# Kernel tuning notes

Hardware: AMD Instinct MI355X
Metric: run time of the kernel (lower is better)

The kernel has to match this reference:

```python
import jax, jax.numpy as jnp
from jax import lax
import numpy as np

B, NW, L, E, H, V = 8192, 4, 16, 128, 128, 64  # batch, words/example, max chars, emsize, hidden, char vocab


def setup_inputs() -> dict:
    key = jax.random.key(0)
    ks = jax.random.split(key, 13)
    s = 0.05
    return {
        "word_ids": jax.random.randint(ks[0], (B, NW, L), 0, V, dtype=jnp.int32),
        "lengths": jax.random.randint(ks[1], (B, NW), 1, L + 1, dtype=jnp.int32),
        "emb_i": jax.random.normal(ks[2], (V, E), jnp.float32),
        "W_ih": jax.random.normal(ks[3], (4 * H, E), jnp.float32) * s,
        "W_hh": jax.random.normal(ks[4], (4 * H, H), jnp.float32) * s,
        "b_ih": jax.random.normal(ks[5], (4 * H,), jnp.float32) * s,
        "b_hh": jax.random.normal(ks[6], (4 * H,), jnp.float32) * s,
        "conv1_w": jax.random.normal(ks[7], (4, 1, 2, 2), jnp.float32) * 0.5,
        "conv1_b": jax.random.normal(ks[8], (4,), jnp.float32) * 0.1,
        "conv2_w": jax.random.normal(ks[9], (8, 4, 2, 2), jnp.float32) * 0.5,
        "conv2_b": jax.random.normal(ks[10], (8,), jnp.float32) * 0.1,
        "scorer_w": jax.random.normal(ks[11], (1, 2 * 2 * 8), jnp.float32) * 0.2,
        "scorer_b": jax.random.normal(ks[12], (1,), jnp.float32) * 0.1,
    }


def reference(word_ids, lengths, emb_i, W_ih, W_hh, b_ih, b_hh,
              conv1_w, conv1_b, conv2_w, conv2_b, scorer_w, scorer_b):
    Bx, NWx, Lx = word_ids.shape
    Hh = W_hh.shape[1]
    BN = Bx * NWx
    # char embeddings for all words, packed: [L, BN, E]
    xs = emb_i[word_ids.reshape(BN, Lx)].transpose(1, 0, 2)
    # ragged lengths -> per-step update mask [L, BN]
    mask = jnp.arange(Lx, dtype=lengths.dtype)[:, None] < lengths.reshape(-1)[None, :]
    h0 = jnp.zeros((BN, Hh), emb_i.dtype)

    def step(carry, xm):
        h, c = carry
        x_t, m = xm
        gates = x_t @ W_ih.T + b_ih + h @ W_hh.T + b_hh  # torch LSTMCell gate order i,f,g,o
        i, f, g, o = jnp.split(gates, 4, axis=-1)
        i = jax.nn.sigmoid(i); f = jax.nn.sigmoid(f)
        g = jnp.tanh(g); o = jax.nn.sigmoid(o)
        c_new = f * c + i * g
        h_new = o * jnp.tanh(c_new)
        m = m[:, None]
        return (jnp.where(m, h_new, h), jnp.where(m, c_new, c)), None

    (h, c), _ = lax.scan(step, (h0, h0), (xs, mask))
    # Model.encode returns the cell state c
    reps = c.reshape(Bx, NWx, Hh)

    # pairwise cosine similarity matrix [B, NW, NW]
    norms = jnp.sqrt(jnp.sum(reps * reps, axis=-1))
    dots = jnp.einsum('bih,bjh->bij', reps, reps)
    cos = dots / (norms[:, :, None] * norms[:, None, :])

    # tiny 2-layer CNN scorer on the NWxNW matrix (NCHW)
    dn = ('NCHW', 'OIHW', 'NCHW')
    x_img = cos[:, None, :, :]
    out = jax.nn.relu(lax.conv_general_dilated(x_img, conv1_w, (1, 1), 'VALID', dimension_numbers=dn)
                      + conv1_b[None, :, None, None])
    out = jax.nn.relu(lax.conv_general_dilated(out, conv2_w, (1, 1), 'VALID', dimension_numbers=dn)
                      + conv2_b[None, :, None, None])
    flat = out.reshape(Bx, -1)  # channel-major flatten matches torch .view
    score = flat @ scorer_w.T + scorer_b
    return jax.nn.sigmoid(score)  # [B, 1] discriminator prob
```

## Files before the change

kernel.cpp:

```cpp
#include <hip/hip_runtime.h>

#define BSZ    8192
#define NWRD   4
#define SEQL   16
#define HDIM   128
#define VOCAB  64
#define NSEQ   (BSZ * NWRD)
#define WGSEQ  32
#define UPB    80
#define BINCAP (UPB * WGSEQ)
#define NBLK   512
#define RSTR   136

#define AS1 __attribute__((address_space(1)))
#define AS3 __attribute__((address_space(3)))

typedef float    f32x4  __attribute__((ext_vector_type(4)));
typedef float    f32x16 __attribute__((ext_vector_type(16)));
typedef __bf16   bf16x8 __attribute__((ext_vector_type(8)));
typedef _Float16 f16x8  __attribute__((ext_vector_type(8)));
typedef int      i32x4  __attribute__((ext_vector_type(4)));

union AccU { f32x16 v; f32x4 q[4]; float f[16]; };

__device__ __forceinline__ unsigned short f2bf(float f) {
    unsigned int u = __builtin_bit_cast(unsigned int, f);
    return (unsigned short)((u + 0x7fff + ((u >> 16) & 1)) >> 16);
}
__device__ __forceinline__ float sigm(float x) {
    return __builtin_amdgcn_rcpf(1.f + __builtin_amdgcn_exp2f(x * -1.44269504f));
}

__global__ void prep4(const float* __restrict__ emb, const float* __restrict__ W_ih,
                      const float* __restrict__ b_ih, const float* __restrict__ b_hh,
                      const float* __restrict__ W_hh, const int* __restrict__ lengths,
                      unsigned short* __restrict__ P2H, unsigned short* __restrict__ WA,
                      int* __restrict__ perm, int* __restrict__ gh)
{
    __shared__ int lh[16], gbase[16];
    const int blk = blockIdx.x, tid = threadIdx.x;

    if (blk < 128) {
        int idx = blk * 256 + tid;
        int v = idx >> 9, g = (idx >> 7) & 3, j = idx & 127;
        int n = g * 128 + j;
        const f32x4* er = (const f32x4*)(emb  + v * 128);
        const f32x4* wr = (const f32x4*)(W_ih + n * 128);
        f32x4 s4 = er[0] * wr[0];
#pragma unroll
        for (int e = 1; e < 32; ++e) s4 += er[e] * wr[e];
        float s = s4.x + s4.y + s4.z + s4.w + b_ih[n] + b_hh[n];
        int wv = j >> 5, jr = j & 31;
        int d = jr & 3, hl = (jr >> 2) & 1, q = jr >> 3;
        int cc = g * 16 + wv * 4 + hl * 2 + (q >> 1);
        int F  = v * 512 + ((cc ^ (v & 7)) << 3) + (q & 1) * 4 + d;
        P2H[F] = __builtin_bit_cast(unsigned short, (_Float16)s);
    } else if (blk < 384) {
        int idx = (blk - 128) * 256 + tid;
        int jj = idx & 7, lane = (idx >> 3) & 63, kc = (idx >> 9) & 7, tt = idx >> 12;
        int wv = tt >> 2, g = tt & 3;
        int n = g * 128 + wv * 32 + (lane & 31);
        int k = kc * 16 + (lane >> 5) * 8 + jj;
        WA[idx] = f2bf(W_hh[n * 128 + k]);
    } else {
        if (tid < 16) lh[tid] = 0;
        __syncthreads();
        int i = (blk - 384) * 256 + tid;
        int b = 16 - lengths[i];
        int rank = atomicAdd(&lh[b], 1);
        __syncthreads();
        if (tid < 16) gbase[tid] = atomicAdd(&gh[tid], lh[tid]);
        __syncthreads();
        perm[b * BINCAP + gbase[b] + rank] = i;
    }
}

__global__ __launch_bounds__(256, 2) void lstm4(
    const int* __restrict__ word_ids, const int* __restrict__ perm,
    int* __restrict__ gh, const unsigned short* __restrict__ P2H,
    const unsigned short* __restrict__ WA, float* __restrict__ c_out)
{
    __shared__ __align__(16) unsigned short ptab[VOCAB * 512];
    __shared__ __align__(16) unsigned short hbuf[2][WGSEQ * 128];

    const int tid    = threadIdx.x;
    const int wv     = tid >> 6;
    const int lane   = tid & 63;
    const int lane31 = lane & 31;
    const int hl     = lane >> 5;

    {
        const char* src = (const char*)P2H;
        char*       dst = (char*)ptab;
#pragma unroll
        for (int r = 0; r < 16; ++r) {
            const int off = r * 4096 + wv * 1024;
            __builtin_amdgcn_global_load_lds(
                (const AS1 unsigned int*)(src + off + lane * 16),
                (AS3 unsigned int*)(dst + off), 16, 0, 0);
        }
    }

    bf16x8 afr[4][8];
#pragma unroll
    for (int g = 0; g < 4; ++g)
#pragma unroll
        for (int kc = 0; kc < 8; ++kc)
            afr[g][kc] = *(const bf16x8*)(WA + (((wv * 4 + g) * 8 + kc) * 64 + lane) * 8);

    int ghs[16];
#pragma unroll
    for (int i = 0; i < 16; ++i)
        ghs[i] = __builtin_amdgcn_readfirstlane(gh[i]);
    int tot = 0;
#pragma unroll
    for (int i = 0; i < 16; ++i) tot += (ghs[i] + 31) >> 5;

    const int      rdo_b = lane31 * 256;
    const unsigned xv    = (unsigned)((lane31 & 7) << 4);
    const int      jbase = wv * 32 + 4 * hl;
    const int      ccb   = wv * 4 + hl * 2;
    int* const tick_p = (int*)&hbuf[0][0];

    for (;;) {
        __syncthreads();
        if (tid == 0) *tick_p = atomicAdd(gh + 16, 1);
        __syncthreads();
        const int k = *tick_p;
        if (k >= tot) break;

        int rem = k, bsel = 0, found = 0;
#pragma unroll
        for (int b2 = 0; b2 < 16; ++b2) {
            int nb = (ghs[b2] + 31) >> 5;
            if (!found) {
                if (rem < nb) { bsel = b2; found = 1; }
                else rem -= nb;
            }
        }
        const int widx = rem;
        const int cnt  = ghs[bsel];
        const int ml   = 16 - bsel;

        const int slot = widx * WGSEQ + lane31;
        const int live = slot < cnt;
        const int sid  = live ? perm[bsel * BINCAP + slot] : 0;
        unsigned long long u0, u1;
        {
            const i32x4* wp = (const i32x4*)(word_ids + sid * SEQL);
            i32x4 a = wp[0], b4 = wp[1], c4 = wp[2], d4 = wp[3];
            unsigned lo0 = (unsigned)(a.x  | (a.y  << 8) | (a.z  << 16) | (a.w  << 24));
            unsigned hi0 = (unsigned)(b4.x | (b4.y << 8) | (b4.z << 16) | (b4.w << 24));
            unsigned lo1 = (unsigned)(c4.x | (c4.y << 8) | (c4.z << 16) | (c4.w << 24));
            unsigned hi1 = (unsigned)(d4.x | (d4.y << 8) | (d4.z << 16) | (d4.w << 24));
            u0 = ((unsigned long long)hi0 << 32) | lo0;
            u1 = ((unsigned long long)hi1 << 32) | lo1;
        }

        f32x4 cq[4] = {{0,0,0,0},{0,0,0,0},{0,0,0,0},{0,0,0,0}};

#pragma unroll 1
        for (int t = 0; t < ml; ++t) {
            const int w = (int)(u0 & 63);
            u0 = (u0 >> 8) | (u1 << 56); u1 >>= 8;

            AccU acc[4];
            {
                const char*    rowp = (const char*)ptab + (w << 10);
                const unsigned wx   = (unsigned)((w & 7) << 4);
#pragma unroll
                for (int g = 0; g < 4; ++g)
#pragma unroll
                    for (int s = 0; s < 2; ++s) {
                        const unsigned off =
                            ((unsigned)((g * 16 + ccb + s) << 4)) ^ wx;
                        f16x8 hv = *(const f16x8*)(rowp + off);
#pragma unroll
                        for (int kk = 0; kk < 8; ++kk)
                            acc[g].f[s * 8 + kk] = (float)hv[kk];
                    }
            }

            if (t > 0) {
                const char* hr = (const char*)hbuf[t & 1];
                bf16x8 bfv[8];
#pragma unroll
                for (int kc = 0; kc < 8; ++kc)
                    bfv[kc] = *(const bf16x8*)(hr + rdo_b +
                                  (((unsigned)(kc * 32 + hl * 16)) ^ xv));
#pragma unroll
                for (int kc = 0; kc < 8; ++kc) {
                    const bf16x8 bb = bfv[kc];
#pragma unroll
                    for (int g = 0; g < 4; ++g)
                        acc[g].v = __builtin_amdgcn_mfma_f32_32x32x16_bf16(
                            afr[g][kc], bb, acc[g].v, 0, 0, 0);
                }
            }

            const int wr = (t < ml - 1);
            char* hw = (char*)hbuf[(t + 1) & 1];
#pragma unroll
            for (int q = 0; q < 4; ++q) {
                float hv4[4];
#pragma unroll
                for (int d = 0; d < 4; ++d) {
                    const int r = q * 4 + d;
                    float ei = __builtin_amdgcn_exp2f(acc[0].f[r] * -1.44269504f);
                    float ef = __builtin_amdgcn_exp2f(acc[1].f[r] * -1.44269504f);
                    float eg = __builtin_amdgcn_exp2f(acc[2].f[r] *  2.88539008f);
                    float ai = 1.f + ei, af = 1.f + ef, ag = 1.f + eg;
                    float t1 = ai * ag;
                    float R  = __builtin_amdgcn_rcpf(t1 * af);
                    float cn = __builtin_fmaf(cq[q][d], t1, (eg - 1.f) * af) * R;
                    cq[q][d] = cn;
                    if (wr) {
                        float eo = __builtin_amdgcn_exp2f(acc[3].f[r] * -1.44269504f);
                        float ec = __builtin_amdgcn_exp2f(cn * 2.88539008f);
                        hv4[d] = (ec - 1.f) *
                                 __builtin_amdgcn_rcpf((1.f + eo) * (1.f + ec));
                    }
                }
                if (wr) {
                    unsigned int plo_, phi_;
                    asm("v_cvt_pk_bf16_f32 %0, %1, %2"
                        : "=v"(plo_) : "v"(hv4[0]), "v"(hv4[1]));
                    asm("v_cvt_pk_bf16_f32 %0, %1, %2"
                        : "=v"(phi_) : "v"(hv4[2]), "v"(hv4[3]));
                    unsigned long long pu_ =
                        ((unsigned long long)phi_ << 32) | plo_;
                    *(unsigned long long*)(hw + rdo_b +
                        (((unsigned)(wv * 64 + q * 16)) ^ xv) + hl * 8) = pu_;
                }
            }
            if (wr) __syncthreads();
        }

        if (live) {
#pragma unroll
            for (int q = 0; q < 4; ++q)
                *(f32x4*)(c_out + sid * HDIM + jbase + 8 * q) = cq[q];
        }
    }
}

__global__ __launch_bounds__(256) void epilogue(
    const float* __restrict__ c_ws,
    const float* __restrict__ conv1_w, const float* __restrict__ conv1_b,
    const float* __restrict__ conv2_w, const float* __restrict__ conv2_b,
    const float* __restrict__ scorer_w, const float* __restrict__ scorer_b,
    float* __restrict__ out)
{
    __shared__ __align__(16) float reps[8 * NWRD * RSTR];
    __shared__ float gram_s[8 * 16];

    const int tid = threadIdx.x;
    const int b0  = blockIdx.x * 8;

    for (int i = tid; i < 8 * NWRD * HDIM; i += 256)
        reps[(i >> 7) * RSTR + (i & 127)] = c_ws[b0 * NWRD * HDIM + i];
    __syncthreads();

    const int bt  = tid >> 5;
    const int sub = tid & 31;

    float dval = 0.f;
    if (sub < 16) {
        int i = sub >> 2, j = sub & 3;
        const f32x4* ci = (const f32x4*)(reps + (bt * 4 + i) * RSTR);
        const f32x4* cj = (const f32x4*)(reps + (bt * 4 + j) * RSTR);
        f32x4 s4 = {0.f, 0.f, 0.f, 0.f};
        for (int k = 0; k < HDIM / 4; ++k) s4 += ci[k] * cj[k];
        dval = s4.x + s4.y + s4.z + s4.w;
        gram_s[bt * 16 + sub] = dval;
    }
    __syncthreads();
    float cosv = 0.f;
    if (sub < 16) {
        int i = sub >> 2, j = sub & 3;
        float di = gram_s[bt * 16 + i * 4 + i];
        float dj = gram_s[bt * 16 + j * 4 + j];
        cosv = __fdividef(dval, sqrtf(di * dj));
    }
    __syncthreads();
    if (sub < 16) gram_s[bt * 16 + sub] = cosv;
    __syncthreads();

    if (sub == 0) {
        float img[4][4];
#pragma unroll
        for (int i = 0; i < 4; ++i)
#pragma unroll
            for (int j = 0; j < 4; ++j) img[i][j] = gram_s[bt * 16 + i * 4 + j];

        float o1[4][3][3];
#pragma unroll
        for (int ch = 0; ch < 4; ++ch) {
            float w00 = conv1_w[ch*4+0], w01 = conv1_w[ch*4+1];
            float w10 = conv1_w[ch*4+2], w11 = conv1_w[ch*4+3];
            float bb  = conv1_b[ch];
#pragma unroll
            for (int y = 0; y < 3; ++y)
#pragma unroll
                for (int x = 0; x < 3; ++x) {
                    float s = bb + w00*img[y][x]   + w01*img[y][x+1]
                                 + w10*img[y+1][x] + w11*img[y+1][x+1];
                    o1[ch][y][x] = s > 0.f ? s : 0.f;
                }
        }
        float sc = scorer_b[0];
#pragma unroll
        for (int oc = 0; oc < 8; ++oc) {
            float bb = conv2_b[oc];
#pragma unroll
            for (int y = 0; y < 2; ++y)
#pragma unroll
                for (int x = 0; x < 2; ++x) {
                    float s = bb;
#pragma unroll
                    for (int ic = 0; ic < 4; ++ic) {
                        const float* w = conv2_w + oc * 16 + ic * 4;
                        s += w[0]*o1[ic][y][x]   + w[1]*o1[ic][y][x+1]
                           + w[2]*o1[ic][y+1][x] + w[3]*o1[ic][y+1][x+1];
                    }
                    float rl = s > 0.f ? s : 0.f;
                    sc += rl * scorer_w[oc * 4 + y * 2 + x];
                }
        }
        out[blockIdx.x * 8 + bt] = sigm(sc);
    }
}

extern "C" void kernel_launch(void* const* d_in, const int* in_sizes, int n_in,
                              void* d_out, int out_size, void* d_ws, size_t ws_size,
                              hipStream_t stream)
{
    const int*   word_ids = (const int*)d_in[0];
    const int*   lengths  = (const int*)d_in[1];
    const float* emb      = (const float*)d_in[2];
    const float* W_ih     = (const float*)d_in[3];
    const float* W_hh     = (const float*)d_in[4];
    const float* b_ih     = (const float*)d_in[5];
    const float* b_hh     = (const float*)d_in[6];
    const float* conv1_w  = (const float*)d_in[7];
    const float* conv1_b  = (const float*)d_in[8];
    const float* conv2_w  = (const float*)d_in[9];
    const float* conv2_b  = (const float*)d_in[10];
    const float* scorer_w = (const float*)d_in[11];
    const float* scorer_b = (const float*)d_in[12];
    float* out = (float*)d_out;

    char* ws = (char*)d_ws;
    unsigned short* P2H  = (unsigned short*)(ws + 0);
    unsigned short* WA   = (unsigned short*)(ws + (128<<10));
    int*            perm = (int*)(ws + (256<<10));
    int*            gh   = (int*)(ws + (416<<10));
    float*          c_ws = (float*)(ws + (512<<10));

    hipMemsetAsync(gh, 0, 17 * sizeof(int), stream);
    prep4   <<<512,  256, 0, stream>>>(emb, W_ih, b_ih, b_hh, W_hh, lengths,
                                       P2H, WA, perm, gh);
    lstm4   <<<NBLK, 256, 0, stream>>>(word_ids, perm, gh, P2H, WA, c_ws);
    epilogue<<<BSZ / 8, 256, 0, stream>>>(c_ws, conv1_w, conv1_b, conv2_w, conv2_b,
                                          scorer_w, scorer_b, out);
}
```

Before: 165.6 us.

## Switch LSTM recurrence to 16x16x32 MFMA with 8 waves per block

Replaces the 32x32x16 bf16 MFMA recurrent matmul with 16x16x32 MFMAs and doubles the workgroup to 512 threads, so each wave owns 16 hidden units for two 16-sequence halves. The W_hh fragment layout and the gate-table layout built in prep are rearranged to match, and each lane now tracks two sequences. The aim is to spread each timestep's work over more waves, which halves the per-wave weight registers and the serial MFMA chain between barriers. In exchange the barrier spans 8 waves and twice as many MFMA issues are needed.

```diff
diff --git a/kernel.cpp b/kernel.cpp
--- a/kernel.cpp
+++ b/kernel.cpp
@@ -16,12 +16,9 @@
 #define AS3 __attribute__((address_space(3)))
 
 typedef float    f32x4  __attribute__((ext_vector_type(4)));
-typedef float    f32x16 __attribute__((ext_vector_type(16)));
 typedef __bf16   bf16x8 __attribute__((ext_vector_type(8)));
-typedef _Float16 f16x8  __attribute__((ext_vector_type(8)));
+typedef _Float16 f16x4  __attribute__((ext_vector_type(4)));
 typedef int      i32x4  __attribute__((ext_vector_type(4)));
-
-union AccU { f32x16 v; f32x4 q[4]; float f[16]; };
 
 __device__ __forceinline__ unsigned short f2bf(float f) {
     unsigned int u = __builtin_bit_cast(unsigned int, f);
@@ -50,17 +47,15 @@
 #pragma unroll
         for (int e = 1; e < 32; ++e) s4 += er[e] * wr[e];
         float s = s4.x + s4.y + s4.z + s4.w + b_ih[n] + b_hh[n];
-        int wv = j >> 5, jr = j & 31;
-        int d = jr & 3, hl = (jr >> 2) & 1, q = jr >> 3;
-        int cc = g * 16 + wv * 4 + hl * 2 + (q >> 1);
-        int F  = v * 512 + ((cc ^ (v & 7)) << 3) + (q & 1) * 4 + d;
+        int qidx = g * 32 + (j >> 2);
+        int F = v * 512 + (((qidx << 2) + (j & 3)) ^ ((v & 7) << 3));
         P2H[F] = __builtin_bit_cast(unsigned short, (_Float16)s);
     } else if (blk < 384) {
         int idx = (blk - 128) * 256 + tid;
-        int jj = idx & 7, lane = (idx >> 3) & 63, kc = (idx >> 9) & 7, tt = idx >> 12;
+        int jj = idx & 7, lane = (idx >> 3) & 63, kc = (idx >> 9) & 3, tt = idx >> 11;
         int wv = tt >> 2, g = tt & 3;
-        int n = g * 128 + wv * 32 + (lane & 31);
-        int k = kc * 16 + (lane >> 5) * 8 + jj;
+        int n = g * 128 + wv * 16 + (lane & 15);
+        int k = kc * 32 + ((lane >> 4) & 3) * 8 + jj;
         WA[idx] = f2bf(W_hh[n * 128 + k]);
     } else {
         if (tid < 16) lh[tid] = 0;
@@ -75,7 +70,7 @@
     }
 }
 
-__global__ __launch_bounds__(256, 2) void lstm4(
+__global__ __launch_bounds__(512, 4) void lstm4(
     const int* __restrict__ word_ids, const int* __restrict__ perm,
     int* __restrict__ gh, const unsigned short* __restrict__ P2H,
     const unsigned short* __restrict__ WA, float* __restrict__ c_out)
@@ -83,30 +78,30 @@
     __shared__ __align__(16) unsigned short ptab[VOCAB * 512];
     __shared__ __align__(16) unsigned short hbuf[2][WGSEQ * 128];
 
-    const int tid    = threadIdx.x;
-    const int wv     = tid >> 6;
-    const int lane   = tid & 63;
-    const int lane31 = lane & 31;
-    const int hl     = lane >> 5;
+    const int tid  = threadIdx.x;
+    const int wv   = tid >> 6;
+    const int lane = tid & 63;
+    const int l15  = lane & 15;
+    const int hi   = (lane >> 4) & 3;
 
     {
         const char* src = (const char*)P2H;
         char*       dst = (char*)ptab;
 #pragma unroll
-        for (int r = 0; r < 16; ++r) {
-            const int off = r * 4096 + wv * 1024;
+        for (int r = 0; r < 8; ++r) {
+            const int off = (wv * 8 + r) * 1024;
             __builtin_amdgcn_global_load_lds(
                 (const AS1 unsigned int*)(src + off + lane * 16),
                 (AS3 unsigned int*)(dst + off), 16, 0, 0);
         }
     }
 
-    bf16x8 afr[4][8];
+    bf16x8 afr[4][4];
 #pragma unroll
     for (int g = 0; g < 4; ++g)
 #pragma unroll
-        for (int kc = 0; kc < 8; ++kc)
-            afr[g][kc] = *(const bf16x8*)(WA + (((wv * 4 + g) * 8 + kc) * 64 + lane) * 8);
+        for (int kc = 0; kc < 4; ++kc)
+            afr[g][kc] = *(const bf16x8*)(WA + (((wv * 4 + g) * 4 + kc) * 64 + lane) * 8);
 
     int ghs[16];
 #pragma unroll
@@ -116,10 +111,9 @@
 #pragma unroll
     for (int i = 0; i < 16; ++i) tot += (ghs[i] + 31) >> 5;
 
-    const int      rdo_b = lane31 * 256;
-    const unsigned xv    = (unsigned)((lane31 & 7) << 4);
-    const int      jbase = wv * 32 + 4 * hl;
-    const int      ccb   = wv * 4 + hl * 2;
+    const unsigned xv  = (unsigned)((l15 & 7) << 4);
+    const int      jql = wv * 16 + hi * 4;
+    const unsigned pqb = (unsigned)((jql >> 2) * 8);
     int* const tick_p = (int*)&hbuf[0][0];
 
     for (;;) {
@@ -142,80 +136,95 @@
         const int cnt  = ghs[bsel];
         const int ml   = 16 - bsel;
 
-        const int slot = widx * WGSEQ + lane31;
-        const int live = slot < cnt;
-        const int sid  = live ? perm[bsel * BINCAP + slot] : 0;
-        unsigned long long u0, u1;
+        const int slot0 = widx * WGSEQ + l15;
+        const int slot1 = slot0 + 16;
+        const int live0 = slot0 < cnt;
+        const int live1 = slot1 < cnt;
+        const int sid0  = live0 ? perm[bsel * BINCAP + slot0] : 0;
+        const int sid1  = live1 ? perm[bsel * BINCAP + slot1] : 0;
+
+        unsigned long long u0a, u1a, u0b, u1b;
         {
-            const i32x4* wp = (const i32x4*)(word_ids + sid * SEQL);
+            const i32x4* wp = (const i32x4*)(word_ids + sid0 * SEQL);
             i32x4 a = wp[0], b4 = wp[1], c4 = wp[2], d4 = wp[3];
-            unsigned lo0 = (unsigned)(a.x  | (a.y  << 8) | (a.z  << 16) | (a.w  << 24));
-            unsigned hi0 = (unsigned)(b4.x | (b4.y << 8) | (b4.z << 16) | (b4.w << 24));
-            unsigned lo1 = (unsigned)(c4.x | (c4.y << 8) | (c4.z << 16) | (c4.w << 24));
-            unsigned hi1 = (unsigned)(d4.x | (d4.y << 8) | (d4.z << 16) | (d4.w << 24));
-            u0 = ((unsigned long long)hi0 << 32) | lo0;
-            u1 = ((unsigned long long)hi1 << 32) | lo1;
-        }
-
-        f32x4 cq[4] = {{0,0,0,0},{0,0,0,0},{0,0,0,0},{0,0,0,0}};
+            u0a = ((unsigned long long)(unsigned)(b4.x | (b4.y << 8) | (b4.z << 16) | (b4.w << 24)) << 32)
+                |  (unsigned)(a.x  | (a.y  << 8) | (a.z  << 16) | (a.w  << 24));
+            u1a = ((unsigned long long)(unsigned)(d4.x | (d4.y << 8) | (d4.z << 16) | (d4.w << 24)) << 32)
+                |  (unsigned)(c4.x | (c4.y << 8) | (c4.z << 16) | (c4.w << 24));
+        }
+        {
+            const i32x4* wp = (const i32x4*)(word_ids + sid1 * SEQL);
+            i32x4 a = wp[0], b4 = wp[1], c4 = wp[2], d4 = wp[3];
+            u0b = ((unsigned long long)(unsigned)(b4.x | (b4.y << 8) | (b4.z << 16) | (b4.w << 24)) << 32)
+                |  (unsigned)(a.x  | (a.y  << 8) | (a.z  << 16) | (a.w  << 24));
+            u1b = ((unsigned long long)(unsigned)(d4.x | (d4.y << 8) | (d4.z << 16) | (d4.w << 24)) << 32)
+                |  (unsigned)(c4.x | (c4.y << 8) | (c4.z << 16) | (c4.w << 24));
+        }
+
+        f32x4 cq0 = {0,0,0,0}, cq1 = {0,0,0,0};
 
 #pragma unroll 1
         for (int t = 0; t < ml; ++t) {
-            const int w = (int)(u0 & 63);
-            u0 = (u0 >> 8) | (u1 << 56); u1 >>= 8;
-
-            AccU acc[4];
+            const int w0 = (int)(u0a & 63);
+            u0a = (u0a >> 8) | (u1a << 56); u1a >>= 8;
+            const int w1 = (int)(u0b & 63);
+            u0b = (u0b >> 8) | (u1b << 56); u1b >>= 8;
+
+            f32x4 acc[4][2];
             {
-                const char*    rowp = (const char*)ptab + (w << 10);
-                const unsigned wx   = (unsigned)((w & 7) << 4);
-#pragma unroll
-                for (int g = 0; g < 4; ++g)
-#pragma unroll
-                    for (int s = 0; s < 2; ++s) {
-                        const unsigned off =
-                            ((unsigned)((g * 16 + ccb + s) << 4)) ^ wx;
-                        f16x8 hv = *(const f16x8*)(rowp + off);
-#pragma unroll
-                        for (int kk = 0; kk < 8; ++kk)
-                            acc[g].f[s * 8 + kk] = (float)hv[kk];
+                const char*    r0  = (const char*)ptab + (w0 << 10);
+                const unsigned wx0 = (unsigned)((w0 & 7) << 4);
+                const char*    r1  = (const char*)ptab + (w1 << 10);
+                const unsigned wx1 = (unsigned)((w1 & 7) << 4);
+#pragma unroll
+                for (int g = 0; g < 4; ++g) {
+                    const unsigned bo = (unsigned)(g * 256) + pqb;
+                    f16x4 p0 = *(const f16x4*)(r0 + (bo ^ wx0));
+                    f16x4 p1 = *(const f16x4*)(r1 + (bo ^ wx1));
+#pragma unroll
+                    for (int d = 0; d < 4; ++d) {
+                        acc[g][0][d] = (float)p0[d];
+                        acc[g][1][d] = (float)p1[d];
                     }
+                }
             }
 
             if (t > 0) {
                 const char* hr = (const char*)hbuf[t & 1];
-                bf16x8 bfv[8];
-#pragma unroll
-                for (int kc = 0; kc < 8; ++kc)
-                    bfv[kc] = *(const bf16x8*)(hr + rdo_b +
-                                  (((unsigned)(kc * 32 + hl * 16)) ^ xv));
-#pragma unroll
-                for (int kc = 0; kc < 8; ++kc) {
-                    const bf16x8 bb = bfv[kc];
-#pragma unroll
-                    for (int g = 0; g < 4; ++g)
-                        acc[g].v = __builtin_amdgcn_mfma_f32_32x32x16_bf16(
-                            afr[g][kc], bb, acc[g].v, 0, 0, 0);
+                const int row0 = l15 * 256, row1 = row0 + 16 * 256;
+#pragma unroll
+                for (int kc = 0; kc < 4; ++kc) {
+                    const unsigned ko = (unsigned)(kc * 64 + hi * 16);
+                    bf16x8 b0 = *(const bf16x8*)(hr + row0 + (ko ^ xv));
+                    bf16x8 b1 = *(const bf16x8*)(hr + row1 + (ko ^ xv));
+#pragma unroll
+                    for (int g = 0; g < 4; ++g) {
+                        acc[g][0] = __builtin_amdgcn_mfma_f32_16x16x32_bf16(
+                            afr[g][kc], b0, acc[g][0], 0, 0, 0);
+                        acc[g][1] = __builtin_amdgcn_mfma_f32_16x16x32_bf16(
+                            afr[g][kc], b1, acc[g][1], 0, 0, 0);
+                    }
                 }
             }
 
             const int wr = (t < ml - 1);
             char* hw = (char*)hbuf[(t + 1) & 1];
 #pragma unroll
-            for (int q = 0; q < 4; ++q) {
+            for (int st = 0; st < 2; ++st) {
                 float hv4[4];
 #pragma unroll
                 for (int d = 0; d < 4; ++d) {
-                    const int r = q * 4 + d;
-                    float ei = __builtin_amdgcn_exp2f(acc[0].f[r] * -1.44269504f);
-                    float ef = __builtin_amdgcn_exp2f(acc[1].f[r] * -1.44269504f);
-                    float eg = __builtin_amdgcn_exp2f(acc[2].f[r] *  2.88539008f);
+                    float cprev = st ? cq1[d] : cq0[d];
+                    float ei = __builtin_amdgcn_exp2f(acc[0][st][d] * -1.44269504f);
+                    float ef = __builtin_amdgcn_exp2f(acc[1][st][d] * -1.44269504f);
+                    float eg = __builtin_amdgcn_exp2f(acc[2][st][d] *  2.88539008f);
                     float ai = 1.f + ei, af = 1.f + ef, ag = 1.f + eg;
                     float t1 = ai * ag;
                     float R  = __builtin_amdgcn_rcpf(t1 * af);
-                    float cn = __builtin_fmaf(cq[q][d], t1, (eg - 1.f) * af) * R;
-                    cq[q][d] = cn;
+                    float cn = __builtin_fmaf(cprev, t1, (eg - 1.f) * af) * R;
+                    if (st) cq1[d] = cn; else cq0[d] = cn;
                     if (wr) {
-                        float eo = __builtin_amdgcn_exp2f(acc[3].f[r] * -1.44269504f);
+                        float eo = __builtin_amdgcn_exp2f(acc[3][st][d] * -1.44269504f);
                         float ec = __builtin_amdgcn_exp2f(cn * 2.88539008f);
                         hv4[d] = (ec - 1.f) *
                                  __builtin_amdgcn_rcpf((1.f + eo) * (1.f + ec));
@@ -229,18 +238,15 @@
                         : "=v"(phi_) : "v"(hv4[2]), "v"(hv4[3]));
                     unsigned long long pu_ =
                         ((unsigned long long)phi_ << 32) | plo_;
-                    *(unsigned long long*)(hw + rdo_b +
-                        (((unsigned)(wv * 64 + q * 16)) ^ xv) + hl * 8) = pu_;
+                    *(unsigned long long*)(hw + (st * 16 + l15) * 256 +
+                        (((unsigned)(jql * 2)) ^ xv)) = pu_;
                 }
             }
             if (wr) __syncthreads();
         }
 
-        if (live) {
-#pragma unroll
-            for (int q = 0; q < 4; ++q)
-                *(f32x4*)(c_out + sid * HDIM + jbase + 8 * q) = cq[q];
-        }
+        if (live0) *(f32x4*)(c_out + sid0 * HDIM + jql) = cq0;
+        if (live1) *(f32x4*)(c_out + sid1 * HDIM + jql) = cq1;
     }
 }
 
@@ -360,7 +366,7 @@
     hipMemsetAsync(gh, 0, 17 * sizeof(int), stream);
     prep4   <<<512,  256, 0, stream>>>(emb, W_ih, b_ih, b_hh, W_hh, lengths,
                                        P2H, WA, perm, gh);
-    lstm4   <<<NBLK, 256, 0, stream>>>(word_ids, perm, gh, P2H, WA, c_ws);
+    lstm4   <<<NBLK, 512, 0, stream>>>(word_ids, perm, gh, P2H, WA, c_ws);
     epilogue<<<BSZ / 8, 256, 0, stream>>>(c_ws, conv1_w, conv1_b, conv2_w, conv2_b,
                                           scorer_w, scorer_b, out);
 }
```

New measurement: 171.6 us. 3.7% more time.
